# Performance work log

Hardware: AMD Instinct MI355X
Metric: run time of the kernel (lower is better)

Reference implementation:

```python
import jax, jax.numpy as jnp
import numpy as np

CHUNK = 128
TAU = 0.7


def setup_inputs() -> dict:
    key = jax.random.key(0)
    ks = jax.random.split(key, 8)
    B, S, D, H, E = 4, 4096, 2048, 1024, 8
    x = jax.random.normal(ks[0], (B, S, D), dtype=jnp.float32)
    prev_expert_indices = jax.random.randint(ks[1], (B,), 0, E)
    # router MLP params (stored as [in, out]); xavier-uniform-like init, zero biases
    def xavier(k, fin, fout):
        lim = np.sqrt(6.0 / (fin + fout)).astype(np.float32)
        return jax.random.uniform(k, (fin, fout), jnp.float32, -lim, lim)
    w1 = xavier(ks[2], D, H)
    b1 = jnp.zeros((H,), jnp.float32)
    w2 = xavier(ks[3], H, H // 2)
    b2 = jnp.zeros((H // 2,), jnp.float32)
    w3 = jax.random.normal(ks[4], (H // 2, E), jnp.float32) * 0.02  # final layer std=0.02
    b3 = jnp.zeros((E,), jnp.float32)
    return {"x": x, "prev_expert_indices": prev_expert_indices,
            "w1": w1, "b1": b1, "w2": w2, "b2": b2, "w3": w3, "b3": b3}


def reference(x, prev_expert_indices, w1, b1, w2, b2, w3, b3):
    B, S, D = x.shape
    E = w3.shape[1]
    C = S // CHUNK  # num_chunks (seq_len divisible by chunk_size)

    # Router MLP on every token (Dropout is identity in eval), then per-chunk mean
    h = jax.nn.relu(x @ w1 + b1)
    h = jax.nn.relu(h @ w2 + b2)
    tok_logits = h @ w3 + b3                                   # [B, S, E]
    chunk_logits = tok_logits.reshape(B, C, CHUNK, E).mean(2)  # [B, C, E]

    top = jnp.argmax(chunk_logits, axis=-1).astype(jnp.int32)  # [B, C]

    # Sequential hysteresis over chunks (prev_expert_indices given => hysteresis active)
    def step(prev, inp):
        logits_c, top_c, is_first = inp  # [B,E], [B], scalar bool
        cur = jnp.take_along_axis(logits_c, top_c[:, None], axis=1)[:, 0]
        pv = jnp.take_along_axis(logits_c, prev[:, None], axis=1)[:, 0]
        switch = (cur - pv) > TAU
        final = jnp.where(is_first, top_c, jnp.where(switch, top_c, prev))
        flips = jnp.where(is_first, 0, switch.sum().astype(jnp.int32))
        return final, (final, flips)

    is_first = jnp.arange(C) == 0
    _, (experts_t, flips_t) = jax.lax.scan(
        step, jnp.zeros((B,), jnp.int32),
        (chunk_logits.transpose(1, 0, 2), top.T, is_first))
    expert_indices = experts_t.T                               # [B, C]

    one_hot = jax.nn.one_hot(expert_indices, E, dtype=jnp.float32)  # [B, C, E]
    routing_weights = jnp.broadcast_to(one_hot[:, :, None, :],
                                       (B, C, CHUNK, E)).reshape(B, S, E)

    # Stats
    probs = jax.nn.softmax(chunk_logits, axis=-1)
    gate_entropy = -(probs * jnp.log(probs + 1e-8)).sum(-1).mean()
    expert_utilization = one_hot.mean((0, 1))                  # [E]
    flip_rate = flips_t.sum().astype(jnp.float32) / (B * max(1, C - 1))
    routing_concentration = jnp.linalg.norm(expert_utilization)

    return (routing_weights, expert_indices, chunk_logits,
            gate_entropy, expert_utilization, flip_rate, routing_concentration)
```

## Files before the change

kernel.cpp:

```cpp
#include <hip/hip_runtime.h>
#include <math.h>

typedef _Float16 half_t;
typedef __attribute__((ext_vector_type(4))) _Float16 half4v;
typedef __attribute__((ext_vector_type(8))) _Float16 half8v;
typedef __attribute__((ext_vector_type(4))) float floatx4;

constexpr int B_ = 4, S_ = 4096, D_ = 2048, H_ = 1024, H2_ = 512, E_ = 8;
constexpr int CHUNK_ = 128;
constexpr int C_ = S_ / CHUNK_;
constexpr int M_ = B_ * S_;
constexpr float TAU_ = 0.7f;
constexpr float WSCALE = 64.0f, OSCALE = 1.0f / 64.0f;

constexpr int OUT_RW = 0;
constexpr int OUT_EI = OUT_RW + B_ * S_ * E_;
constexpr int OUT_CL = OUT_EI + B_ * C_;
constexpr int OUT_GE = OUT_CL + B_ * C_ * E_;
constexpr int OUT_UT = OUT_GE + 1;
constexpr int OUT_FR = OUT_UT + E_;
constexpr int OUT_RC = OUT_FR + 1;

__global__ __launch_bounds__(256)
void prep_kernel(const float* __restrict__ x, const float* __restrict__ w1,
                 const float* __restrict__ w2,
                 half_t* __restrict__ xh, half_t* __restrict__ w1t,
                 half_t* __restrict__ w2th, half_t* __restrict__ w2tl,
                 float* __restrict__ cl_acc)
{
    __shared__ float tile[32][33];
    const int tx = threadIdx.x & 31;
    const int ty = threadIdx.x >> 5;
    const int bid = blockIdx.x;

    if (bid < 8192) {
        const int base = bid * 1024 + threadIdx.x;
#pragma unroll
        for (int p = 0; p < 4; ++p) {
            const int i = base + p * 256;
            const float4 v = ((const float4*)x)[i];
            half4v h;
            h.x = (half_t)v.x; h.y = (half_t)v.y; h.z = (half_t)v.z; h.w = (half_t)v.w;
            ((half4v*)xh)[i] = h;
        }
    } else if (bid < 10240) {
        const int b2 = bid - 8192;
        const int n0 = (b2 & 31) * 32;
        const int k0 = (b2 >> 5) * 32;
#pragma unroll
        for (int r = 0; r < 4; ++r)
            tile[ty + r * 8][tx] = w1[(size_t)(k0 + ty + r * 8) * H_ + n0 + tx];
        __syncthreads();
#pragma unroll
        for (int r = 0; r < 4; ++r)
            w1t[(size_t)(n0 + ty + r * 8) * D_ + k0 + tx] = (half_t)tile[tx][ty + r * 8];
    } else if (bid < 10752) {
        const int b2 = bid - 10240;
        const int n0 = (b2 & 15) * 32;
        const int k0 = (b2 >> 4) * 32;
#pragma unroll
        for (int r = 0; r < 4; ++r)
            tile[ty + r * 8][tx] = w2[(size_t)(k0 + ty + r * 8) * H2_ + n0 + tx];
        __syncthreads();
#pragma unroll
        for (int r = 0; r < 4; ++r) {
            const float v = tile[tx][ty + r * 8] * WSCALE;
            const half_t h = (half_t)v;
            const size_t off = (size_t)(n0 + ty + r * 8) * H_ + k0 + tx;
            w2th[off] = h;
            w2tl[off] = (half_t)(v - (float)h);
        }
    } else {
        for (int i = threadIdx.x; i < B_ * C_ * E_; i += 256) cl_acc[i] = 0.0f;
    }
}

__device__ __forceinline__ int lds_off_g(int row, int q)
{
    const int line = row >> 1;
    const int sl = (((row & 1) << 2) | q) ^ (line & 7);
    return line * 64 + sl * 8;
}

__device__ __forceinline__ void stage_half_g1(const half_t* __restrict__ g,
                                              half_t* l, int tid)
{
    const int s = tid & 7;
#pragma unroll
    for (int r = 0; r < 2; ++r) {
        const int line = r * 64 + (tid >> 3);
        const int u = s ^ (line & 7);
        const int row = line * 2 + (u >> 2);
        const int kq = (u & 3) * 8;
        __builtin_amdgcn_global_load_lds(
            (const __attribute__((address_space(1))) void*)(g + (size_t)row * D_ + kq),
            (__attribute__((address_space(3))) void*)(l + (r * 512 + tid) * 8),
            16, 0, 0);
    }
}

__global__ __launch_bounds__(512, 2)
void gemm1_kernel(const half_t* __restrict__ Ah,
                  const half_t* __restrict__ BTh,
                  const float* __restrict__ bias, half_t* __restrict__ outh)
{
    constexpr int KD = D_;
    constexpr int ND = H_;
    constexpr int NT = KD / 64;

    __shared__ __align__(16) half_t sA[2][2][256 * 32];
    __shared__ __align__(16) half_t sB[2][2][256 * 32];

    const int tid = threadIdx.x;
    const int lane = tid & 63;
    const int wave = tid >> 6;
    const int wRow = (wave >> 2) * 128;
    const int wCol = (wave & 3) * 64;
    const int fr = lane & 15;
    const int q = lane >> 4;

    const int bid = blockIdx.x;
    const long blockM = (long)((bid & 7) * 8 + (bid >> 5)) * 256;
    const long blockN = (long)((bid >> 3) & 3) * 256;

    const half_t* gA = Ah + (size_t)blockM * KD;
    const half_t* gB = BTh + (size_t)blockN * KD;

    floatx4 acc[8][4];
#pragma unroll
    for (int i = 0; i < 8; ++i)
#pragma unroll
        for (int j = 0; j < 4; ++j) acc[i][j] = (floatx4){0.f, 0.f, 0.f, 0.f};

    stage_half_g1(gA,      sA[0][0], tid);
    stage_half_g1(gB,      sB[0][0], tid);
    stage_half_g1(gA + 32, sA[0][1], tid);
    stage_half_g1(gB + 32, sB[0][1], tid);
    stage_half_g1(gB + 64, sB[1][0], tid);
    stage_half_g1(gA + 64, sA[1][0], tid);
    stage_half_g1(gB + 96, sB[1][1], tid);
    asm volatile("s_waitcnt vmcnt(6)" ::: "memory");
    __builtin_amdgcn_s_barrier();
    __builtin_amdgcn_sched_barrier(0);

    half8v bfr[4];

#define G1_PHASE(BUF, H, MB, STAGE_STMT, TAIL_STMT)                            \
    {                                                                          \
        half8v afr[4];                                                         \
        if ((MB) == 0) {                                                       \
            _Pragma("unroll")                                                  \
            for (int n = 0; n < 4; ++n)                                        \
                bfr[n] = *(const half8v*)(sB[BUF][H] +                         \
                          lds_off_g(wCol + n * 16 + fr, q));                   \
        }                                                                      \
        _Pragma("unroll")                                                      \
        for (int m = 0; m < 4; ++m)                                            \
            afr[m] = *(const half8v*)(sA[BUF][H] +                             \
                      lds_off_g(wRow + (MB) + m * 16 + fr, q));                \
        STAGE_STMT;                                                            \
        __builtin_amdgcn_s_barrier();                                          \
        asm volatile("s_waitcnt lgkmcnt(0)" ::: "memory");                     \
        __builtin_amdgcn_sched_barrier(0);                                     \
        __builtin_amdgcn_s_setprio(1);                                         \
        _Pragma("unroll")                                                      \
        for (int m = 0; m < 4; ++m)                                            \
            _Pragma("unroll")                                                  \
            for (int n = 0; n < 4; ++n)                                        \
                acc[(MB) / 16 + m][n] = __builtin_amdgcn_mfma_f32_16x16x32_f16(\
                    afr[m], bfr[n], acc[(MB) / 16 + m][n], 0, 0, 0);           \
        __builtin_amdgcn_s_setprio(0);                                         \
        TAIL_STMT;                                                             \
        __builtin_amdgcn_s_barrier();                                          \
        __builtin_amdgcn_sched_barrier(0);                                     \
    }

#define G1_TILE(BUF, T)                                                        \
    {                                                                          \
        G1_PHASE(BUF, 0, 0,                                                    \
            if ((T) + 1 < NT)                                                  \
                stage_half_g1(gA + ((T) + 1) * 64 + 32, sA[(BUF) ^ 1][1], tid),\
            );                                                                 \
        G1_PHASE(BUF, 0, 64,                                                   \
            if ((T) + 2 < NT)                                                  \
                stage_half_g1(gB + ((T) + 2) * 64, sB[BUF][0], tid),           \
            );                                                                 \
        G1_PHASE(BUF, 1, 0,                                                    \
            if ((T) + 2 < NT)                                                  \
                stage_half_g1(gA + ((T) + 2) * 64, sA[BUF][0], tid),           \
            );                                                                 \
        G1_PHASE(BUF, 1, 64,                                                   \
            if ((T) + 2 < NT)                                                  \
                stage_half_g1(gB + ((T) + 2) * 64 + 32, sB[BUF][1], tid),      \
            if ((T) < NT - 2) {                                                \
                asm volatile("s_waitcnt vmcnt(6)" ::: "memory");               \
            } else if ((T) == NT - 2) {                                        \
                asm volatile("s_waitcnt vmcnt(0)" ::: "memory");               \
            });                                                                \
    }

    for (int t = 0; t < NT; t += 2) {
        G1_TILE(0, t);
        G1_TILE(1, t + 1);
    }
#undef G1_TILE
#undef G1_PHASE

    const int orow = (lane >> 4) * 4;
    const int ocol = lane & 15;
#pragma unroll
    for (int n = 0; n < 4; ++n) {
        const long gn = blockN + wCol + n * 16 + ocol;
        const float bj = bias[gn];
#pragma unroll
        for (int m = 0; m < 8; ++m) {
#pragma unroll
            for (int r = 0; r < 4; ++r) {
                const float v = fmaxf(acc[m][n][r] + bj, 0.0f);
                outh[(size_t)(blockM + wRow + m * 16 + orow + r) * ND + gn] = (half_t)v;
            }
        }
    }
}

__global__ __launch_bounds__(256, 3)
void gemm2_fused_kernel(const half_t* __restrict__ Ah,
                        const half_t* __restrict__ BTh, const half_t* __restrict__ BTl,
                        const float* __restrict__ bias, const float* __restrict__ w3,
                        float* __restrict__ cl_acc)
{
    constexpr int KD = H_, BK = 32;
    __shared__ __align__(16) half_t sAh[128 * BK];
    __shared__ __align__(16) half_t sBh[128 * BK];
    __shared__ __align__(16) half_t sBl[128 * BK];

    const int tid = threadIdx.x;
    const int lane = tid & 63;
    const int wave = tid >> 6;
    const int wm = (wave & 1) * 64;
    const int wn = (wave >> 1) * 64;
    const int d = blockIdx.y * 4 + blockIdx.x;
    const int xcd = d & 7;
    const int l = d >> 3;
    const int rowBlk = xcd * 16 + (l >> 2);
    const int colBlk = l & 3;
    const long blockM = (long)rowBlk * 128;
    const long blockN = (long)colBlk * 128;

    floatx4 acc[4][4];
#pragma unroll
    for (int i = 0; i < 4; ++i)
#pragma unroll
        for (int j = 0; j < 4; ++j) acc[i][j] = (floatx4){0.f, 0.f, 0.f, 0.f};

    const int srow = tid >> 2;
    const int skoff = (tid & 3) * 8;
    const int ldsoff = srow * BK + skoff;
    const int fr = lane & 15;
    const int fq = (lane >> 4) * 8;

    for (int k0 = 0; k0 < KD; k0 += BK) {
        __syncthreads();
#pragma unroll
        for (int p = 0; p < 2; ++p) {
            const int row = srow + p * 64;
            const size_t aoff = (size_t)(blockM + row) * KD + k0 + skoff;
            const size_t boff = (size_t)(blockN + row) * KD + k0 + skoff;
            const int loff = ldsoff + p * 2048;
            __builtin_amdgcn_global_load_lds(
                (const __attribute__((address_space(1))) void*)(Ah + aoff),
                (__attribute__((address_space(3))) void*)(sAh + loff), 16, 0, 0);
            __builtin_amdgcn_global_load_lds(
                (const __attribute__((address_space(1))) void*)(BTh + boff),
                (__attribute__((address_space(3))) void*)(sBh + loff), 16, 0, 0);
            __builtin_amdgcn_global_load_lds(
                (const __attribute__((address_space(1))) void*)(BTl + boff),
                (__attribute__((address_space(3))) void*)(sBl + loff), 16, 0, 0);
        }
        __syncthreads();

        half8v fbh[4], fbl[4];
#pragma unroll
        for (int t = 0; t < 4; ++t) {
            fbh[t] = *(const half8v*)(sBh + (wn + t * 16 + fr) * BK + fq);
            fbl[t] = *(const half8v*)(sBl + (wn + t * 16 + fr) * BK + fq);
        }
#pragma unroll
        for (int i = 0; i < 4; ++i) {
            const half8v fah = *(const half8v*)(sAh + (wm + i * 16 + fr) * BK + fq);
#pragma unroll
            for (int j = 0; j < 4; ++j) {
                acc[i][j] = __builtin_amdgcn_mfma_f32_16x16x32_f16(fah, fbh[j], acc[i][j], 0, 0, 0);
                acc[i][j] = __builtin_amdgcn_mfma_f32_16x16x32_f16(fah, fbl[j], acc[i][j], 0, 0, 0);
            }
        }
    }

    const int ocol = lane & 15;
    float p[E_];
#pragma unroll
    for (int e = 0; e < E_; ++e) p[e] = 0.0f;
#pragma unroll
    for (int j = 0; j < 4; ++j) {
        const int gn = (int)blockN + wn + j * 16 + ocol;
        const float bj = bias[gn];
        const float4 w3a = *(const float4*)(w3 + (size_t)gn * E_);
        const float4 w3b = *(const float4*)(w3 + (size_t)gn * E_ + 4);
        float colsum = 0.0f;
#pragma unroll
        for (int i = 0; i < 4; ++i)
#pragma unroll
            for (int r = 0; r < 4; ++r)
                colsum += fmaxf(acc[i][j][r] * OSCALE + bj, 0.0f);
        p[0] += colsum * w3a.x; p[1] += colsum * w3a.y;
        p[2] += colsum * w3a.z; p[3] += colsum * w3a.w;
        p[4] += colsum * w3b.x; p[5] += colsum * w3b.y;
        p[6] += colsum * w3b.z; p[7] += colsum * w3b.w;
    }
#pragma unroll
    for (int e = 0; e < E_; ++e)
#pragma unroll
        for (int off = 32; off > 0; off >>= 1)
            p[e] += __shfl_xor(p[e], off);
#pragma unroll
    for (int e = 0; e < E_; ++e)
        if (lane == e) atomicAdd(&cl_acc[rowBlk * E_ + e], p[e]);
}

__global__ __launch_bounds__(256)
void final_route_kernel(const float* __restrict__ cl_acc, const float* __restrict__ b3,
                        float* __restrict__ out)
{
    __shared__ float cl[B_ * C_][E_];
    __shared__ int tops[B_ * C_];
    __shared__ int finals[B_ * C_];
    __shared__ int flips[B_];
    __shared__ float ent[B_ * C_];

    const int tid = threadIdx.x;

    if (tid < B_ * C_) {
        int best = 0;
        float bvv = -1e30f;
#pragma unroll
        for (int e = 0; e < E_; ++e) {
            const float v = cl_acc[tid * E_ + e] * (1.0f / CHUNK_) + b3[e];
            cl[tid][e] = v;
            if (v > bvv) { bvv = v; best = e; }
        }
        tops[tid] = best;
    }
    __syncthreads();

    if (tid < B_) {
        const int b = tid;
        int prev = 0, fl = 0;
        for (int c = 0; c < C_; ++c) {
            const int t = tops[b * C_ + c];
            int fin;
            if (c == 0) {
                fin = t;
            } else {
                const float cur = cl[b * C_ + c][t];
                const float pv = cl[b * C_ + c][prev];
                const bool sw = (cur - pv) > TAU_;
                if (sw) fl++;
                fin = sw ? t : prev;
            }
            finals[b * C_ + c] = fin;
            prev = fin;
        }
        flips[b] = fl;
    }
    __syncthreads();

    {
        const int tok = blockIdx.x * 256 + tid;
        const int b = tok >> 12;
        const int c = (tok & (S_ - 1)) >> 7;
        const int e = finals[b * C_ + c];
        float4 v0 = make_float4(e == 0 ? 1.f : 0.f, e == 1 ? 1.f : 0.f,
                                e == 2 ? 1.f : 0.f, e == 3 ? 1.f : 0.f);
        float4 v1 = make_float4(e == 4 ? 1.f : 0.f, e == 5 ? 1.f : 0.f,
                                e == 6 ? 1.f : 0.f, e == 7 ? 1.f : 0.f);
        float4* dst = (float4*)(out + OUT_RW + (size_t)tok * E_);
        dst[0] = v0;
        dst[1] = v1;
    }

    if (blockIdx.x == 0) {
        if (tid < B_ * C_) {
            out[OUT_EI + tid] = (float)finals[tid];
#pragma unroll
            for (int e = 0; e < E_; ++e) out[OUT_CL + tid * E_ + e] = cl[tid][e];
            float m = cl[tid][0];
            for (int e = 1; e < E_; ++e) m = fmaxf(m, cl[tid][e]);
            float pr[E_], s = 0.0f;
            for (int e = 0; e < E_; ++e) { pr[e] = expf(cl[tid][e] - m); s += pr[e]; }
            const float inv = 1.0f / s;
            float h = 0.0f;
            for (int e = 0; e < E_; ++e) { const float pe = pr[e] * inv; h -= pe * logf(pe + 1e-8f); }
            ent[tid] = h;
        }
        __syncthreads();
        if (tid == 0) {
            float esum = 0.0f;
            for (int i = 0; i < B_ * C_; ++i) esum += ent[i];
            out[OUT_GE] = esum / (float)(B_ * C_);

            int cnt[E_];
            for (int e = 0; e < E_; ++e) cnt[e] = 0;
            for (int i = 0; i < B_ * C_; ++i) cnt[finals[i]]++;
            float n2 = 0.0f;
            for (int e = 0; e < E_; ++e) {
                const float u = (float)cnt[e] / (float)(B_ * C_);
                out[OUT_UT + e] = u;
                n2 += u * u;
            }
            const int totfl = flips[0] + flips[1] + flips[2] + flips[3];
            out[OUT_FR] = (float)totfl / (float)(B_ * (C_ - 1));
            out[OUT_RC] = sqrtf(n2);
        }
    }
}

extern "C" void kernel_launch(void* const* d_in, const int* in_sizes, int n_in,
                              void* d_out, int out_size, void* d_ws, size_t ws_size,
                              hipStream_t stream)
{
    const float* x  = (const float*)d_in[0];
    const float* w1 = (const float*)d_in[2];
    const float* b1 = (const float*)d_in[3];
    const float* w2 = (const float*)d_in[4];
    const float* b2 = (const float*)d_in[5];
    const float* w3 = (const float*)d_in[6];
    const float* b3 = (const float*)d_in[7];
    float* out = (float*)d_out;

    half_t* xh   = (half_t*)d_ws;
    half_t* w1t  = xh + (size_t)M_ * D_;
    half_t* h1h  = w1t + (size_t)H_ * D_;
    half_t* w2th = h1h + (size_t)M_ * H_;
    half_t* w2tl = w2th + (size_t)H2_ * H_;
    float*  cl_acc = (float*)(w2tl + (size_t)H2_ * H_);

    prep_kernel<<<dim3(10753), dim3(256), 0, stream>>>(x, w1, w2, xh, w1t, w2th, w2tl, cl_acc);
    gemm1_kernel<<<dim3(256), dim3(512), 0, stream>>>(xh, w1t, b1, h1h);
    gemm2_fused_kernel<<<dim3(H2_ / 128, M_ / 128), dim3(256), 0, stream>>>(
        h1h, w2th, w2tl, b2, w3, cl_acc);
    final_route_kernel<<<dim3(M_ / 256), dim3(256), 0, stream>>>(cl_acc, b3, out);
}
```

Baseline: 346.0 us.

## Double-buffer LDS fragment reads across GEMM1 phases with partial lgkmcnt waits

Restructures the first GEMM's main loop so that LDS reads of A/B fragments for the next phase are issued before the current phase's MFMAs, using two register slots per fragment. The lgkmcnt(0) wait and one barrier per phase are replaced by partial lgkmcnt/vmcnt waits tuned to the new issue order. The goal is to hide LDS read latency behind MFMA work. In exchange it uses more VGPRs and depends on fragile hand-counted wait values that could race if they are wrong.

```diff
diff --git a/kernel.cpp b/kernel.cpp
--- a/kernel.cpp
+++ b/kernel.cpp
@@ -132,6 +132,27 @@
 #pragma unroll
         for (int j = 0; j < 4; ++j) acc[i][j] = (floatx4){0.f, 0.f, 0.f, 0.f};
 
+    half8v afr2[2][4];
+    half8v bfr2[2][4];
+
+#define G1_VM(N)   asm volatile("s_waitcnt vmcnt(" #N ")" ::: "memory")
+#define G1_LGKM(N) asm volatile("s_waitcnt lgkmcnt(" #N ")" ::: "memory")
+
+#define RD_A(BUFi, Hi, MBv, SL)                                                \
+    do {                                                                       \
+        afr2[SL][0] = *(const half8v*)(sA[BUFi][Hi] + lds_off_g(wRow + (MBv) + 0 + fr, q));  \
+        afr2[SL][1] = *(const half8v*)(sA[BUFi][Hi] + lds_off_g(wRow + (MBv) + 16 + fr, q)); \
+        afr2[SL][2] = *(const half8v*)(sA[BUFi][Hi] + lds_off_g(wRow + (MBv) + 32 + fr, q)); \
+        afr2[SL][3] = *(const half8v*)(sA[BUFi][Hi] + lds_off_g(wRow + (MBv) + 48 + fr, q)); \
+    } while (0)
+#define RD_B(BUFi, Hi, SL)                                                     \
+    do {                                                                       \
+        bfr2[SL][0] = *(const half8v*)(sB[BUFi][Hi] + lds_off_g(wCol + 0 + fr, q));  \
+        bfr2[SL][1] = *(const half8v*)(sB[BUFi][Hi] + lds_off_g(wCol + 16 + fr, q)); \
+        bfr2[SL][2] = *(const half8v*)(sB[BUFi][Hi] + lds_off_g(wCol + 32 + fr, q)); \
+        bfr2[SL][3] = *(const half8v*)(sB[BUFi][Hi] + lds_off_g(wCol + 48 + fr, q)); \
+    } while (0)
+
     stage_half_g1(gA,      sA[0][0], tid);
     stage_half_g1(gB,      sB[0][0], tid);
     stage_half_g1(gA + 32, sA[0][1], tid);
@@ -139,36 +160,25 @@
     stage_half_g1(gB + 64, sB[1][0], tid);
     stage_half_g1(gA + 64, sA[1][0], tid);
     stage_half_g1(gB + 96, sB[1][1], tid);
-    asm volatile("s_waitcnt vmcnt(6)" ::: "memory");
+    G1_VM(10);
     __builtin_amdgcn_s_barrier();
     __builtin_amdgcn_sched_barrier(0);
-
-    half8v bfr[4];
-
-#define G1_PHASE(BUF, H, MB, STAGE_STMT, TAIL_STMT)                            \
+    RD_B(0, 0, 0);
+    RD_A(0, 0, 0, 0);
+
+#define G1_PHASE(RD_STMT, STAGE_STMT, LGKM_STMT, FA, FB, MBv, TAIL_STMT)       \
     {                                                                          \
-        half8v afr[4];                                                         \
-        if ((MB) == 0) {                                                       \
-            _Pragma("unroll")                                                  \
-            for (int n = 0; n < 4; ++n)                                        \
-                bfr[n] = *(const half8v*)(sB[BUF][H] +                         \
-                          lds_off_g(wCol + n * 16 + fr, q));                   \
-        }                                                                      \
-        _Pragma("unroll")                                                      \
-        for (int m = 0; m < 4; ++m)                                            \
-            afr[m] = *(const half8v*)(sA[BUF][H] +                             \
-                      lds_off_g(wRow + (MB) + m * 16 + fr, q));                \
+        RD_STMT;                                                               \
         STAGE_STMT;                                                            \
-        __builtin_amdgcn_s_barrier();                                          \
-        asm volatile("s_waitcnt lgkmcnt(0)" ::: "memory");                     \
+        LGKM_STMT;                                                             \
         __builtin_amdgcn_sched_barrier(0);                                     \
         __builtin_amdgcn_s_setprio(1);                                         \
         _Pragma("unroll")                                                      \
         for (int m = 0; m < 4; ++m)                                            \
             _Pragma("unroll")                                                  \
             for (int n = 0; n < 4; ++n)                                        \
-                acc[(MB) / 16 + m][n] = __builtin_amdgcn_mfma_f32_16x16x32_f16(\
-                    afr[m], bfr[n], acc[(MB) / 16 + m][n], 0, 0, 0);           \
+                acc[(MBv) / 16 + m][n] = __builtin_amdgcn_mfma_f32_16x16x32_f16(\
+                    afr2[FA][m], bfr2[FB][n], acc[(MBv) / 16 + m][n], 0, 0, 0);\
         __builtin_amdgcn_s_setprio(0);                                         \
         TAIL_STMT;                                                             \
         __builtin_amdgcn_s_barrier();                                          \
@@ -177,26 +187,29 @@
 
 #define G1_TILE(BUF, T)                                                        \
     {                                                                          \
-        G1_PHASE(BUF, 0, 0,                                                    \
-            if ((T) + 1 < NT)                                                  \
-                stage_half_g1(gA + ((T) + 1) * 64 + 32, sA[(BUF) ^ 1][1], tid),\
-            );                                                                 \
-        G1_PHASE(BUF, 0, 64,                                                   \
-            if ((T) + 2 < NT)                                                  \
-                stage_half_g1(gB + ((T) + 2) * 64, sB[BUF][0], tid),           \
-            );                                                                 \
-        G1_PHASE(BUF, 1, 0,                                                    \
-            if ((T) + 2 < NT)                                                  \
-                stage_half_g1(gA + ((T) + 2) * 64, sA[BUF][0], tid),           \
-            );                                                                 \
-        G1_PHASE(BUF, 1, 64,                                                   \
-            if ((T) + 2 < NT)                                                  \
-                stage_half_g1(gB + ((T) + 2) * 64 + 32, sB[BUF][1], tid),      \
-            if ((T) < NT - 2) {                                                \
-                asm volatile("s_waitcnt vmcnt(6)" ::: "memory");               \
-            } else if ((T) == NT - 2) {                                        \
-                asm volatile("s_waitcnt vmcnt(0)" ::: "memory");               \
-            });                                                                \
+                  \
+        G1_PHASE(RD_A(BUF, 0, 64, 1),                                          \
+            if ((T) + 1 < NT) stage_half_g1(gA + ((T) + 1) * 64 + 32,          \
+                                            sA[(BUF) ^ 1][1], tid),            \
+            G1_LGKM(4), 0, 0, 0,                                               \
+            if ((T) < NT - 1) { G1_VM(8); } else { G1_VM(0); });               \
+         \
+        G1_PHASE(RD_B(BUF, 1, 1); RD_A(BUF, 1, 0, 0),                          \
+            if ((T) + 2 < NT) stage_half_g1(gB + ((T) + 2) * 64,               \
+                                            sB[(BUF)][0], tid),                \
+            G1_LGKM(8), 1, 0, 64, );                                           \
+                  \
+        G1_PHASE(RD_A(BUF, 1, 64, 1),                                          \
+            if ((T) + 2 < NT) stage_half_g1(gA + ((T) + 2) * 64,               \
+                                            sA[(BUF)][0], tid),                \
+            G1_LGKM(4), 0, 1, 0,                                               \
+            if ((T) < NT - 2) { G1_VM(8); } else if ((T) == NT - 2) { G1_VM(4); }); \
+          \
+        G1_PHASE(if ((T) < NT - 1) { RD_B((BUF) ^ 1, 0, 0); RD_A((BUF) ^ 1, 0, 0, 0); }, \
+            if ((T) + 2 < NT) stage_half_g1(gB + ((T) + 2) * 64 + 32,          \
+                                            sB[(BUF)][1], tid),                \
+            if ((T) < NT - 1) { G1_LGKM(8); } else { G1_LGKM(0); },            \
+            1, 1, 64, );                                                       \
     }
 
     for (int t = 0; t < NT; t += 2) {
@@ -205,6 +218,10 @@
     }
 #undef G1_TILE
 #undef G1_PHASE
+#undef RD_A
+#undef RD_B
+#undef G1_VM
+#undef G1_LGKM
 
     const int orow = (lane >> 4) * 4;
     const int ocol = lane & 15;
```

Result: slower. 370.4 us (+7.1%).
